# Kernel tuning notes

Measured on AMD Instinct MI355X. Metric: run time of the kernel, lower is better.

Reference implementation:

```python
import jax, jax.numpy as jnp
import numpy as np

B, S, EMB = 2, 2048, 4096
NHEADS, KVHEADS, HEAD_D = 32, 8, 128
SPLITS = (NHEADS * HEAD_D, KVHEADS * HEAD_D, KVHEADS * HEAD_D)  # 4096, 1024, 1024


def setup_inputs() -> dict:
    key = jax.random.key(0)
    k1, k2, k3 = jax.random.split(key, 3)
    q = jax.random.normal(k1, (B, S, EMB), dtype=jnp.float32)
    # nn.Linear weights, torch layout [out_features, in_features], std=0.02 init
    w_qkv = jax.random.normal(k2, (sum(SPLITS), EMB), dtype=jnp.float32) * 0.02
    w_dense = jax.random.normal(k3, (EMB, NHEADS * HEAD_D), dtype=jnp.float32) * 0.02
    return {"q": q, "w_qkv": w_qkv, "w_dense": w_dense}


def reference(q, w_qkv, w_dense):
    # Self-attention path of PagedMultiHeadAttention (no cache), causal mask.
    Bq, Sq, _ = q.shape
    qkv = q @ w_qkv.T                                  # [B, S, 6144]
    qs, ks, vs = jnp.split(qkv, np.cumsum(SPLITS)[:-1], axis=-1)
    G = NHEADS // KVHEADS                              # GQA expansion = 4
    # queries grouped per kv-head: [B, S, KVH, G, D]
    qh = qs.reshape(Bq, Sq, KVHEADS, G, HEAD_D)
    kh = ks.reshape(Bq, Sq, KVHEADS, HEAD_D)
    vh = vs.reshape(Bq, Sq, KVHEADS, HEAD_D)
    scale = 1.0 / jnp.sqrt(jnp.float32(HEAD_D))
    scores = jnp.einsum("bskgd,btkd->bkgst", qh, kh) * scale  # [B,KVH,G,S,S]
    causal = jnp.tril(jnp.ones((Sq, Sq), dtype=bool))
    scores = jnp.where(causal, scores, jnp.finfo(scores.dtype).min)
    probs = jax.nn.softmax(scores, axis=-1)
    attn = jnp.einsum("bkgst,btkd->bskgd", probs, vh)  # [B,S,KVH,G,D]
    attn = attn.reshape(Bq, Sq, NHEADS * HEAD_D)
    return attn @ w_dense.T                            # [B, S, EMB]
```

## Files before the change

kernel.cpp:

```cpp
#include <hip/hip_runtime.h>
#include <hip/hip_bf16.h>

typedef __bf16 bf16x8 __attribute__((ext_vector_type(8)));
typedef __bf16 bf16x4 __attribute__((ext_vector_type(4)));
typedef float  f32x4  __attribute__((ext_vector_type(4)));

__global__ void cast_f32_bf16(const float* __restrict__ src, __bf16* __restrict__ dst, int n8) {
    int i = blockIdx.x * 256 + threadIdx.x;
    if (i >= n8) return;
    const float4* s = (const float4*)src;
    float4 a = s[2 * i], b = s[2 * i + 1];
    bf16x8 o;
    o[0] = (__bf16)a.x; o[1] = (__bf16)a.y; o[2] = (__bf16)a.z; o[3] = (__bf16)a.w;
    o[4] = (__bf16)b.x; o[5] = (__bf16)b.y; o[6] = (__bf16)b.z; o[7] = (__bf16)b.w;
    ((bf16x8*)dst)[i] = o;
}

template <int OUT_BF16>
__global__ __launch_bounds__(256)
void gemm_bt(const __bf16* __restrict__ A, const __bf16* __restrict__ Bm,
             void* __restrict__ Cout, int M, int N, int K) {
    __shared__ __bf16 As[128 * 64];
    __shared__ __bf16 Bs[128 * 64];
    const int tid = threadIdx.x;
    const int lane = tid & 63, wid = tid >> 6;
    const int g = lane >> 4, lq = lane & 15;
    const int wr = wid >> 1, wc = wid & 1;
    const size_t brow = (size_t)blockIdx.y * 128, bcol = (size_t)blockIdx.x * 128;
    f32x4 acc[4][4] = {};
    const int nkt = K >> 6;

    for (int kt = 0; kt < nkt; ++kt) {
        __syncthreads();
#pragma unroll
        for (int is = 0; is < 4; ++is) {
            int flat = is * 4096 + tid * 16;
            int row  = flat >> 7;
            int colb = flat & 127;
            int sw   = colb ^ ((row & 7) << 4);
            int4 va = *(const int4*)((const char*)A + ((brow + row) * (size_t)K + (size_t)kt * 64) * 2 + colb);
            *(int4*)((char*)As + row * 128 + sw) = va;
            int4 vb = *(const int4*)((const char*)Bm + ((bcol + row) * (size_t)K + (size_t)kt * 64) * 2 + colb);
            *(int4*)((char*)Bs + row * 128 + sw) = vb;
        }
        __syncthreads();
#pragma unroll
        for (int ks = 0; ks < 2; ++ks) {
            bf16x8 af[4], bfr[4];
            const int kb = ks * 64 + g * 16;
#pragma unroll
            for (int i = 0; i < 4; ++i) {
                int row = wr * 64 + i * 16 + lq;
                af[i] = *(const bf16x8*)((const char*)As + row * 128 + (kb ^ ((row & 7) << 4)));
            }
#pragma unroll
            for (int j = 0; j < 4; ++j) {
                int row = wc * 64 + j * 16 + lq;
                bfr[j] = *(const bf16x8*)((const char*)Bs + row * 128 + (kb ^ ((row & 7) << 4)));
            }
#pragma unroll
            for (int i = 0; i < 4; ++i)
#pragma unroll
                for (int j = 0; j < 4; ++j)
                    acc[i][j] = __builtin_amdgcn_mfma_f32_16x16x32_bf16(af[i], bfr[j], acc[i][j], 0, 0, 0);
        }
    }
#pragma unroll
    for (int i = 0; i < 4; ++i) {
#pragma unroll
        for (int r = 0; r < 4; ++r) {
            size_t row = brow + wr * 64 + i * 16 + g * 4 + r;
#pragma unroll
            for (int j = 0; j < 4; ++j) {
                size_t col = bcol + wc * 64 + j * 16 + lq;
                float v = acc[i][j][r];
                if (OUT_BF16) ((__bf16*)Cout)[row * N + col] = (__bf16)v;
                else          ((float*)Cout)[row * N + col] = v;
            }
        }
    }
}

__global__ __launch_bounds__(256)
void transpose_v(const __bf16* __restrict__ qkv, __bf16* __restrict__ vt) {
    constexpr int S = 2048, QKVN = 6144;
    __shared__ __bf16 tile[64][72];
    const int tt = blockIdx.x;
    const int yz = blockIdx.y;
    const int dh = yz & 1, bkh = yz >> 1;
    const int b = bkh >> 3, kh = bkh & 7;
    const int tid = threadIdx.x;
#pragma unroll
    for (int i = 0; i < 2; ++i) {
        int flat = i * 2048 + tid * 8;
        int r = flat >> 6, c0 = flat & 63;
        const __bf16* src = qkv + ((size_t)b * S + tt * 64 + r) * QKVN + 5120 + kh * 128 + dh * 64 + c0;
        *(bf16x8*)&tile[r][c0] = *(const bf16x8*)src;
    }
    __syncthreads();
#pragma unroll
    for (int i = 0; i < 2; ++i) {
        int flat = i * 2048 + tid * 8;
        int d = flat >> 6, t0 = flat & 63;
        bf16x8 pk;
#pragma unroll
        for (int e = 0; e < 8; ++e) pk[e] = tile[t0 + e][d];
        __bf16* dst = vt + ((size_t)(b * 8 + kh) * 128 + dh * 64 + d) * S + tt * 64 + t0;
        *(bf16x8*)dst = pk;
    }
}

__global__ __launch_bounds__(256, 2)
void attn_kernel(const __bf16* __restrict__ qkv, const __bf16* __restrict__ vt,
                 __bf16* __restrict__ outb) {
    constexpr int S = 2048, D = 128, QKVN = 6144;
    const int p = blockIdx.x;
    const int kh = p & 7;
    const int j = p >> 3;
    const int qt = 15 - (j >> 3);
    const int b  = (j >> 2) & 1;
    const int g4 = j & 3;
    const int h  = kh * 4 + g4;
    const int tid = threadIdx.x, lane = tid & 63, w = tid >> 6;
    const int g = lane >> 4, lq = lane & 15;

    __shared__ __bf16 Ks[64 * 128];
    __shared__ __bf16 Vs[128 * 64];
    __shared__ char   PsRaw[4][2][16 * 152];

    const int wqmin = qt * 128 + w * 32;
    const int qg0 = wqmin + lq;
    const int qg1 = qg0 + 16;

    const __bf16* qrow = qkv + ((size_t)(b * S) + wqmin + lq) * QKVN + h * D;
    bf16x8 qf0[4], qf1[4];
#pragma unroll
    for (int ks = 0; ks < 4; ++ks) {
        qf0[ks] = *(const bf16x8*)(qrow + ks * 32 + g * 8);
        qf1[ks] = *(const bf16x8*)(qrow + (size_t)16 * QKVN + ks * 32 + g * 8);
    }

    const char* kbase = (const char*)qkv + ((size_t)(b * S) * QKVN + 4096 + kh * D) * 2;
    const char* vbase = (const char*)vt + ((size_t)(b * 8 + kh) * D * S) * 2;

    f32x4 acc0[8] = {}, acc1[8] = {};
    float m0 = -1e30f, l0 = 0.f, m1 = -1e30f, l1 = 0.f;
    const float scale2 = 0.12753102494f;

    const int krow0 = tid >> 4;
    const int kcolb = (tid & 15) * 16;
    const int vrow0 = tid >> 3;
    const int vcolb = (tid & 7) * 16;

    const int ktmax = 2 * qt + 1;
    int4 pk[4], pv[4];
#pragma unroll
    for (int is = 0; is < 4; ++is) {
        pk[is] = *(const int4*)(kbase + (size_t)(is * 16 + krow0) * QKVN * 2 + kcolb);
        pv[is] = *(const int4*)(vbase + (size_t)(is * 32 + vrow0) * S * 2 + vcolb);
    }

    char* ps0 = &PsRaw[w][0][0];
    char* ps1 = &PsRaw[w][1][0];

    for (int kt = 0; kt <= ktmax; ++kt) {
        __builtin_amdgcn_s_barrier();
#pragma unroll
        for (int is = 0; is < 4; ++is) {
            int row = is * 16 + krow0;
            *(int4*)((char*)Ks + row * 256 + (kcolb ^ ((row & 15) << 4))) = pk[is];
            int d = is * 32 + vrow0;
            *(int4*)((char*)Vs + d * 128 + (vcolb ^ ((d & 7) << 4))) = pv[is];
        }
        if (kt < ktmax) {
#pragma unroll
            for (int is = 0; is < 4; ++is) {
                pk[is] = *(const int4*)(kbase + (size_t)((kt + 1) * 64 + is * 16 + krow0) * QKVN * 2 + kcolb);
                pv[is] = *(const int4*)(vbase + ((size_t)(is * 32 + vrow0) * S + (kt + 1) * 64) * 2 + vcolb);
            }
        }
        __builtin_amdgcn_sched_barrier(0);
        asm volatile("s_waitcnt lgkmcnt(0)" ::: "memory");
        __builtin_amdgcn_sched_barrier(0);
        __builtin_amdgcn_s_barrier();
        __builtin_amdgcn_sched_barrier(0);

        if (kt * 64 <= wqmin + 31) {
            f32x4 sc0[4], sc1[4];
            __builtin_amdgcn_s_setprio(1);
#pragma unroll
            for (int tb = 0; tb < 4; ++tb) {
                f32x4 s0 = {0.f, 0.f, 0.f, 0.f}, s1 = {0.f, 0.f, 0.f, 0.f};
                const int trow = tb * 16 + lq;
                const int rsw = (trow & 15) << 4;
#pragma unroll
                for (int ks = 0; ks < 4; ++ks) {
                    bf16x8 kf = *(const bf16x8*)((const char*)Ks + trow * 256 + ((ks * 64 + g * 16) ^ rsw));
                    s0 = __builtin_amdgcn_mfma_f32_16x16x32_bf16(kf, qf0[ks], s0, 0, 0, 0);
                    s1 = __builtin_amdgcn_mfma_f32_16x16x32_bf16(kf, qf1[ks], s1, 0, 0, 0);
                }
                sc0[tb] = s0; sc1[tb] = s1;
            }
            __builtin_amdgcn_s_setprio(0);

#pragma unroll
            for (int f = 0; f < 2; ++f) {
                f32x4* sc = f ? sc1 : sc0;
                float& m_r = f ? m1 : m0;
                float& l_p = f ? l1 : l0;
                f32x4* acc = f ? acc1 : acc0;
                char* ps = f ? ps1 : ps0;
                const int qg = f ? qg1 : qg0;
                const bool domask = (kt * 64 + 63 > qg - lq);

                float pr[16];
                float rowmax = -1e30f;
#pragma unroll
                for (int tb = 0; tb < 4; ++tb)
#pragma unroll
                    for (int r = 0; r < 4; ++r) {
                        float sv = sc[tb][r] * scale2;
                        if (domask) {
                            int tg = kt * 64 + tb * 16 + g * 4 + r;
                            sv = (tg <= qg) ? sv : -1e30f;
                        }
                        pr[tb * 4 + r] = sv;
                        rowmax = fmaxf(rowmax, sv);
                    }
                rowmax = fmaxf(rowmax, __shfl_xor(rowmax, 16));
                rowmax = fmaxf(rowmax, __shfl_xor(rowmax, 32));
                if (!__all(rowmax - m_r <= 11.0f)) {
                    float m_new = fmaxf(m_r, rowmax);
                    float alpha = exp2f(m_r - m_new);
                    l_p *= alpha;
#pragma unroll
                    for (int r = 0; r < 4; ++r) {
                        float ar = __shfl(alpha, g * 4 + r);
#pragma unroll
                        for (int nb = 0; nb < 8; ++nb) acc[nb][r] *= ar;
                    }
                    m_r = m_new;
                }
                float lsum = 0.f;
#pragma unroll
                for (int i = 0; i < 16; ++i) {
                    float e = exp2f(pr[i] - m_r);
                    pr[i] = e;
                    lsum += e;
                }
                l_p += lsum;
#pragma unroll
                for (int tb = 0; tb < 4; ++tb) {
                    bf16x4 pkv;
#pragma unroll
                    for (int r = 0; r < 4; ++r) pkv[r] = (__bf16)pr[tb * 4 + r];
                    *(bf16x4*)(ps + lq * 152 + tb * 32 + g * 8) = pkv;
                }
            }

            __builtin_amdgcn_s_setprio(1);
#pragma unroll
            for (int ks = 0; ks < 2; ++ks) {
                bf16x8 pa0 = *(const bf16x8*)(ps0 + lq * 152 + ks * 64 + g * 16);
                bf16x8 pa1 = *(const bf16x8*)(ps1 + lq * 152 + ks * 64 + g * 16);
#pragma unroll
                for (int nb = 0; nb < 8; ++nb) {
                    int d = nb * 16 + lq;
                    bf16x8 vf = *(const bf16x8*)((const char*)Vs + d * 128 + ((ks * 64 + g * 16) ^ ((d & 7) << 4)));
                    acc0[nb] = __builtin_amdgcn_mfma_f32_16x16x32_bf16(pa0, vf, acc0[nb], 0, 0, 0);
                    acc1[nb] = __builtin_amdgcn_mfma_f32_16x16x32_bf16(pa1, vf, acc1[nb], 0, 0, 0);
                }
            }
            __builtin_amdgcn_s_setprio(0);
        }
        __builtin_amdgcn_sched_barrier(0);
    }

    l0 += __shfl_xor(l0, 16); l0 += __shfl_xor(l0, 32);
    l1 += __shfl_xor(l1, 16); l1 += __shfl_xor(l1, 32);
    float rl0 = 1.f / l0, rl1 = 1.f / l1;
#pragma unroll
    for (int r = 0; r < 4; ++r) {
        float rr0 = __shfl(rl0, g * 4 + r);
        float rr1 = __shfl(rl1, g * 4 + r);
        size_t row0 = (size_t)(b * S) + wqmin + g * 4 + r;
        __bf16* orow0 = outb + row0 * 4096 + h * D;
        __bf16* orow1 = orow0 + (size_t)16 * 4096;
#pragma unroll
        for (int nb = 0; nb < 8; ++nb) {
            orow0[nb * 16 + lq] = (__bf16)(acc0[nb][r] * rr0);
            orow1[nb * 16 + lq] = (__bf16)(acc1[nb][r] * rr1);
        }
    }
}

extern "C" void kernel_launch(void* const* d_in, const int* in_sizes, int n_in,
                              void* d_out, int out_size, void* d_ws, size_t ws_size,
                              hipStream_t stream) {
    (void)in_sizes; (void)n_in; (void)out_size; (void)ws_size;
    const float* q       = (const float*)d_in[0];
    const float* w_qkv   = (const float*)d_in[1];
    const float* w_dense = (const float*)d_in[2];
    float* out = (float*)d_out;
    char* ws = (char*)d_ws;

    __bf16* qbf      = (__bf16*)(ws);
    __bf16* wqkvbf   = (__bf16*)(ws + 33554432ULL);
    __bf16* wdensebf = (__bf16*)(ws + 83886080ULL);
    __bf16* qkvbf    = (__bf16*)(ws + 117440512ULL);
    __bf16* vtbf     = (__bf16*)(ws + 167772160ULL);
    __bf16* attnbf   = (__bf16*)(ws + 176160768ULL);

    cast_f32_bf16<<<8192, 256, 0, stream>>>(q, qbf, 2097152);
    cast_f32_bf16<<<12288, 256, 0, stream>>>(w_qkv, wqkvbf, 3145728);
    cast_f32_bf16<<<8192, 256, 0, stream>>>(w_dense, wdensebf, 2097152);

    gemm_bt<1><<<dim3(48, 32), 256, 0, stream>>>(qbf, wqkvbf, (void*)qkvbf, 4096, 6144, 4096);
    transpose_v<<<dim3(32, 32), 256, 0, stream>>>(qkvbf, vtbf);
    attn_kernel<<<1024, 256, 0, stream>>>(qkvbf, vtbf, attnbf);
    gemm_bt<0><<<dim3(32, 32), 256, 0, stream>>>(attnbf, wdensebf, (void*)out, 4096, 4096, 4096);
}
```

Before: 705.4 us.

## Replace GEMM with 256x256 double-buffered tile using direct global-to-LDS loads

Both projection GEMMs now use a 512-thread kernel with 256x256 output tiles. Operands are staged straight into LDS with global_load_lds and double buffered, and the next tile's loads are interleaved with the current tile's MFMA work using explicit barriers, waitcnts and setprio. The goal is to raise operand reuse per byte loaded, hide global-memory latency and skip the register round trip when staging. The larger per-thread accumulator and the 128 KB of LDS limit occupancy. The grids get smaller, with only 384 and 256 blocks, which can leave CUs underused.

```diff
diff --git a/kernel.cpp b/kernel.cpp
--- a/kernel.cpp
+++ b/kernel.cpp
@@ -4,6 +4,9 @@
 typedef __bf16 bf16x8 __attribute__((ext_vector_type(8)));
 typedef __bf16 bf16x4 __attribute__((ext_vector_type(4)));
 typedef float  f32x4  __attribute__((ext_vector_type(4)));
+
+typedef __attribute__((address_space(3))) void lds_vp;
+typedef const __attribute__((address_space(1))) void gbl_vp;
 
 __global__ void cast_f32_bf16(const float* __restrict__ src, __bf16* __restrict__ dst, int n8) {
     int i = blockIdx.x * 256 + threadIdx.x;
@@ -16,64 +19,132 @@
     ((bf16x8*)dst)[i] = o;
 }
 
+
+__device__ __forceinline__ void stage_half(const __bf16* __restrict__ g, int K, int kt,
+                                           __bf16* lds_tile, int h, int w, int l) {
+#pragma unroll
+    for (int j = 0; j < 2; ++j) {
+        const int rih = (j * 8 + w) * 8 + (l >> 3);
+        const __bf16* src = g + (size_t)(h * 128 + rih) * K + kt * 64 + (((l & 7) ^ (l >> 3)) << 3);
+        __bf16* dst = lds_tile + h * 8192 + (j * 8 + w) * 512;
+        __builtin_amdgcn_global_load_lds((gbl_vp*)src, (lds_vp*)dst, 16, 0, 0);
+    }
+}
+
+__device__ __forceinline__ bf16x8 lds_frag(const __bf16* base, int row, int kb) {
+    return *(const bf16x8*)((const char*)base + row * 128 + (kb ^ ((row & 7) << 4)));
+}
+
 template <int OUT_BF16>
-__global__ __launch_bounds__(256)
-void gemm_bt(const __bf16* __restrict__ A, const __bf16* __restrict__ Bm,
+__global__ __launch_bounds__(512, 2)
+void gemm256(const __bf16* __restrict__ A, const __bf16* __restrict__ Bm,
              void* __restrict__ Cout, int M, int N, int K) {
-    __shared__ __bf16 As[128 * 64];
-    __shared__ __bf16 Bs[128 * 64];
+    __shared__ __bf16 As[2][256 * 64];
+    __shared__ __bf16 Bs[2][256 * 64];
     const int tid = threadIdx.x;
     const int lane = tid & 63, wid = tid >> 6;
     const int g = lane >> 4, lq = lane & 15;
-    const int wr = wid >> 1, wc = wid & 1;
-    const size_t brow = (size_t)blockIdx.y * 128, bcol = (size_t)blockIdx.x * 128;
-    f32x4 acc[4][4] = {};
-    const int nkt = K >> 6;
-
-    for (int kt = 0; kt < nkt; ++kt) {
-        __syncthreads();
-#pragma unroll
-        for (int is = 0; is < 4; ++is) {
-            int flat = is * 4096 + tid * 16;
-            int row  = flat >> 7;
-            int colb = flat & 127;
-            int sw   = colb ^ ((row & 7) << 4);
-            int4 va = *(const int4*)((const char*)A + ((brow + row) * (size_t)K + (size_t)kt * 64) * 2 + colb);
-            *(int4*)((char*)As + row * 128 + sw) = va;
-            int4 vb = *(const int4*)((const char*)Bm + ((bcol + row) * (size_t)K + (size_t)kt * 64) * 2 + colb);
-            *(int4*)((char*)Bs + row * 128 + sw) = vb;
-        }
-        __syncthreads();
-#pragma unroll
-        for (int ks = 0; ks < 2; ++ks) {
-            bf16x8 af[4], bfr[4];
-            const int kb = ks * 64 + g * 16;
-#pragma unroll
-            for (int i = 0; i < 4; ++i) {
-                int row = wr * 64 + i * 16 + lq;
-                af[i] = *(const bf16x8*)((const char*)As + row * 128 + (kb ^ ((row & 7) << 4)));
-            }
-#pragma unroll
-            for (int j = 0; j < 4; ++j) {
-                int row = wc * 64 + j * 16 + lq;
-                bfr[j] = *(const bf16x8*)((const char*)Bs + row * 128 + (kb ^ ((row & 7) << 4)));
-            }
-#pragma unroll
-            for (int i = 0; i < 4; ++i)
-#pragma unroll
-                for (int j = 0; j < 4; ++j)
-                    acc[i][j] = __builtin_amdgcn_mfma_f32_16x16x32_bf16(af[i], bfr[j], acc[i][j], 0, 0, 0);
-        }
-    }
-#pragma unroll
-    for (int i = 0; i < 4; ++i) {
+    const int wm = wid >> 2, wn = wid & 3;
+    const size_t brow = (size_t)blockIdx.y * 256, bcol = (size_t)blockIdx.x * 256;
+    const __bf16* Ag = A + brow * K;
+    const __bf16* Bg = Bm + bcol * K;
+    const int nkt = K >> 6, niter = nkt >> 1;
+
+    f32x4 acc[8][4] = {};
+
+    stage_half(Ag, K, 0, &As[0][0], 0, wid, lane);
+    stage_half(Bg, K, 0, &Bs[0][0], 0, wid, lane);
+    stage_half(Ag, K, 0, &As[0][0], 1, wid, lane);
+    stage_half(Bg, K, 0, &Bs[0][0], 1, wid, lane);
+
+    const int arow0 = wm * 128 + lq;
+    const int brow0 = wn * 64 + lq;
+
+    for (int it = 0; it < niter; ++it) {
+        const int t0 = 2 * it;
+#pragma unroll
+        for (int hf = 0; hf < 2; ++hf) {
+            const __bf16* SA = &As[hf][0];
+            const __bf16* SB = &Bs[hf][0];
+            __bf16* DA = &As[hf ^ 1][0];
+            __bf16* DB = &Bs[hf ^ 1][0];
+            const int tstage = t0 + 1 + hf;
+            const bool dostage = (tstage < nkt);
+            bf16x8 bfr[4][2];
+
+            if (dostage) stage_half(Ag, K, tstage, DA, 0, wid, lane);
+            __builtin_amdgcn_sched_barrier(0);
+            if (dostage) asm volatile("s_waitcnt vmcnt(2)" ::: "memory");
+            else         asm volatile("s_waitcnt vmcnt(0)" ::: "memory");
+            __builtin_amdgcn_s_barrier();
+            __builtin_amdgcn_sched_barrier(0);
+#pragma unroll
+            for (int n = 0; n < 4; ++n)
+#pragma unroll
+                for (int kk = 0; kk < 2; ++kk)
+                    bfr[n][kk] = lds_frag(SB, brow0 + n * 16, kk * 64 + g * 16);
+            {
+                bf16x8 afr[2][2];
+#pragma unroll
+                for (int mm = 0; mm < 2; ++mm)
+#pragma unroll
+                    for (int kk = 0; kk < 2; ++kk)
+                        afr[mm][kk] = lds_frag(SA, arow0 + mm * 16, kk * 64 + g * 16);
+                __builtin_amdgcn_s_setprio(1);
+#pragma unroll
+                for (int kk = 0; kk < 2; ++kk)
+#pragma unroll
+                    for (int n = 0; n < 4; ++n)
+#pragma unroll
+                        for (int mm = 0; mm < 2; ++mm)
+                            acc[mm][n] = __builtin_amdgcn_mfma_f32_16x16x32_bf16(afr[mm][kk], bfr[n][kk], acc[mm][n], 0, 0, 0);
+                __builtin_amdgcn_s_setprio(0);
+            }
+            __builtin_amdgcn_sched_barrier(0);
+            __builtin_amdgcn_s_barrier();
+            __builtin_amdgcn_sched_barrier(0);
+
+#pragma unroll
+            for (int q = 1; q < 4; ++q) {
+                bf16x8 afr[2][2];
+#pragma unroll
+                for (int mm = 0; mm < 2; ++mm)
+#pragma unroll
+                    for (int kk = 0; kk < 2; ++kk)
+                        afr[mm][kk] = lds_frag(SA, arow0 + (q * 2 + mm) * 16, kk * 64 + g * 16);
+                if (dostage) {
+                    if (q == 1)      stage_half(Bg, K, tstage, DB, 0, wid, lane);
+                    else if (q == 2) stage_half(Ag, K, tstage, DA, 1, wid, lane);
+                    else             stage_half(Bg, K, tstage, DB, 1, wid, lane);
+                }
+                __builtin_amdgcn_sched_barrier(0);
+                __builtin_amdgcn_s_barrier();
+                __builtin_amdgcn_sched_barrier(0);
+                __builtin_amdgcn_s_setprio(1);
+#pragma unroll
+                for (int kk = 0; kk < 2; ++kk)
+#pragma unroll
+                    for (int n = 0; n < 4; ++n)
+#pragma unroll
+                        for (int mm = 0; mm < 2; ++mm)
+                            acc[q * 2 + mm][n] = __builtin_amdgcn_mfma_f32_16x16x32_bf16(afr[mm][kk], bfr[n][kk], acc[q * 2 + mm][n], 0, 0, 0);
+                __builtin_amdgcn_s_setprio(0);
+                __builtin_amdgcn_sched_barrier(0);
+                __builtin_amdgcn_s_barrier();
+                __builtin_amdgcn_sched_barrier(0);
+            }
+        }
+    }
+
+#pragma unroll
+    for (int m = 0; m < 8; ++m) {
 #pragma unroll
         for (int r = 0; r < 4; ++r) {
-            size_t row = brow + wr * 64 + i * 16 + g * 4 + r;
-#pragma unroll
-            for (int j = 0; j < 4; ++j) {
-                size_t col = bcol + wc * 64 + j * 16 + lq;
-                float v = acc[i][j][r];
+            size_t row = brow + wm * 128 + m * 16 + g * 4 + r;
+#pragma unroll
+            for (int n = 0; n < 4; ++n) {
+                size_t col = bcol + wn * 64 + n * 16 + lq;
+                float v = acc[m][n][r];
                 if (OUT_BF16) ((__bf16*)Cout)[row * N + col] = (__bf16)v;
                 else          ((float*)Cout)[row * N + col] = v;
             }
@@ -315,8 +386,8 @@
     cast_f32_bf16<<<12288, 256, 0, stream>>>(w_qkv, wqkvbf, 3145728);
     cast_f32_bf16<<<8192, 256, 0, stream>>>(w_dense, wdensebf, 2097152);
 
-    gemm_bt<1><<<dim3(48, 32), 256, 0, stream>>>(qbf, wqkvbf, (void*)qkvbf, 4096, 6144, 4096);
+    gemm256<1><<<dim3(24, 16), 512, 0, stream>>>(qbf, wqkvbf, (void*)qkvbf, 4096, 6144, 4096);
     transpose_v<<<dim3(32, 32), 256, 0, stream>>>(qkvbf, vtbf);
     attn_kernel<<<1024, 256, 0, stream>>>(qkvbf, vtbf, attnbf);
-    gemm_bt<0><<<dim3(32, 32), 256, 0, stream>>>(attnbf, wdensebf, (void*)out, 4096, 4096, 4096);
-}
+    gemm256<0><<<dim3(16, 16), 512, 0, stream>>>(attnbf, wdensebf, (void*)out, 4096, 4096, 4096);
+}
```

Result: faster. 677.0 us (-4.0%).
